# Kernel optimization log

Hardware: AMD Instinct MI355X
Metric: run time of the kernel (lower is better)

Reference implementation:

```python
import jax, jax.numpy as jnp
import numpy as np

N_NODES = 50000
N_EDGES = 400000
NODE_DIM = 128
EDGE_DIM = 64
HIDDEN = 128  # must equal NODE_DIM (index_add into zeros_like(node_feat))
EPS = 1e-8


def _param(key, shape):
    fan_in = shape[0]
    return (jax.random.normal(key, shape, jnp.float32) / np.sqrt(fan_in)).astype(jnp.float32)


def setup_inputs() -> dict:
    key = jax.random.key(0)
    ks = jax.random.split(key, 20)
    inp = {
        'node_feat': jax.random.normal(ks[0], (N_NODES, NODE_DIM), jnp.float32),
        'edge_attr': jax.random.normal(ks[1], (N_EDGES, EDGE_DIM), jnp.float32),
        'coords': 5.0 * jax.random.normal(ks[2], (N_NODES, 3), jnp.float32),
        'edge_index': jax.random.randint(ks[3], (2, N_EDGES), 0, N_NODES, dtype=jnp.int32),
        # edge_mlp: Linear(2*node+edge -> hidden), SiLU, Linear(hidden -> hidden), SiLU
        'We1': _param(ks[4], (2 * NODE_DIM + EDGE_DIM, HIDDEN)),
        'be1': jnp.zeros((HIDDEN,), jnp.float32),
        'We2': _param(ks[5], (HIDDEN, HIDDEN)),
        'be2': jnp.zeros((HIDDEN,), jnp.float32),
        # node_mlp: Linear(node+hidden -> hidden), SiLU, Linear(hidden -> node)
        'Wn1': _param(ks[6], (NODE_DIM + HIDDEN, HIDDEN)),
        'bn1': jnp.zeros((HIDDEN,), jnp.float32),
        'Wn2': _param(ks[7], (HIDDEN, NODE_DIM)),
        'bn2': jnp.zeros((NODE_DIM,), jnp.float32),
        # coord_mlp: Linear(hidden -> hidden//2), SiLU, Linear(hidden//2 -> 1)
        'Wc1': _param(ks[8], (HIDDEN, HIDDEN // 2)),
        'bc1': jnp.zeros((HIDDEN // 2,), jnp.float32),
        'Wc2': _param(ks[9], (HIDDEN // 2, 1)),
        'bc2': jnp.zeros((1,), jnp.float32),
    }
    return inp


def reference(node_feat, edge_attr, coords, edge_index,
              We1, be1, We2, be2,
              Wn1, bn1, Wn2, bn2,
              Wc1, bc1, Wc2, bc2):
    src, dst = edge_index[0], edge_index[1]
    n_nodes = node_feat.shape[0]

    # gather -> edge MLP
    edge_feat = jnp.concatenate([node_feat[src], node_feat[dst], edge_attr], axis=-1)  # [E, 2*ND+ED]
    edge_message = jax.nn.silu(jax.nn.silu(edge_feat @ We1 + be1) @ We2 + be2)         # [E, H]

    # scatter-add messages to destination nodes
    aggr = jax.ops.segment_sum(edge_message, dst, num_segments=n_nodes)                # [N, H]

    # node update (residual)
    node_in = jnp.concatenate([node_feat, aggr], axis=-1)
    node_update = jax.nn.silu(node_in @ Wn1 + bn1) @ Wn2 + bn2
    updated_nodes = node_feat + node_update

    # equivariant coordinate update
    coord_w = jax.nn.silu(edge_message @ Wc1 + bc1) @ Wc2 + bc2                        # [E, 1]
    coord_diff = coords[src] - coords[dst]                                             # [E, 3]
    coord_diff = coord_diff / (jnp.linalg.norm(coord_diff, axis=-1, keepdims=True) + EPS)
    coord_update = jax.ops.segment_sum(coord_w * coord_diff, dst, num_segments=n_nodes)
    updated_coords = coords + coord_update

    return (updated_nodes, updated_coords)
```

## Files before the change

### kernel.cpp

```cpp
#include <hip/hip_runtime.h>
#include <hip/hip_bf16.h>
#include <math.h>
#include <stdint.h>

#define NN 50000
#define NE 400000

typedef __attribute__((ext_vector_type(8))) short short8;
typedef __attribute__((ext_vector_type(4))) float f32x4;

#define OFF_WE1T 0
#define OFF_WE2T 40960
#define OFF_WN1T 57344
#define OFF_WN2T 90112
#define OFF_WC1T 106496
#define W_TOTAL  114688

#define NFB_ITEMS 800000
#define EAB_ITEMS 3200000

__device__ __forceinline__ float silu_f(float x) {
    return x * (1.0f / (1.0f + __expf(-x)));
}
__device__ __forceinline__ short f2bf(float f) {
    __hip_bfloat16 b = __float2bfloat16(f);
    return *reinterpret_cast<short*>(&b);
}
__device__ __forceinline__ short8 cvt8(float4 a, float4 b) {
    short8 r;
    r[0] = f2bf(a.x); r[1] = f2bf(a.y); r[2] = f2bf(a.z); r[3] = f2bf(a.w);
    r[4] = f2bf(b.x); r[5] = f2bf(b.y); r[6] = f2bf(b.z); r[7] = f2bf(b.w);
    return r;
}

__device__ __forceinline__ void gload16(const short* g, short* l) {
    __builtin_amdgcn_global_load_lds(
        (const __attribute__((address_space(1))) void*)g,
        (__attribute__((address_space(3))) void*)l, 16, 0, 0);
}

__global__ void zero_kernel(float4* __restrict__ p, int n4) {
    int i = blockIdx.x * blockDim.x + threadIdx.x;
    int st = gridDim.x * blockDim.x;
    for (; i < n4; i += st) p[i] = make_float4(0.f, 0.f, 0.f, 0.f);
}

__global__ __launch_bounds__(256) void prep_kernel(
    const float* __restrict__ We1, const float* __restrict__ We2,
    const float* __restrict__ Wn1, const float* __restrict__ Wn2,
    const float* __restrict__ Wc1, const float* __restrict__ nf,
    const float* __restrict__ ea,
    short* __restrict__ wb, short* __restrict__ nfb, short* __restrict__ eab,
    int full)
{
    const int i = blockIdx.x * 256 + threadIdx.x;
    if (i < W_TOTAL) {
        const float* src; int N, n, k, rel;
        if (i < OFF_WE2T)      { rel = i;            src = We1; N = 128; n = rel / 320; k = rel % 320; }
        else if (i < OFF_WN1T) { rel = i - OFF_WE2T; src = We2; N = 128; n = rel / 128; k = rel % 128; }
        else if (i < OFF_WN2T) { rel = i - OFF_WN1T; src = Wn1; N = 128; n = rel / 256; k = rel % 256; }
        else if (i < OFF_WC1T) { rel = i - OFF_WN2T; src = Wn2; N = 128; n = rel / 128; k = rel % 128; }
        else                   { rel = i - OFF_WC1T; src = Wc1; N = 64;  n = rel / 128; k = rel % 128; }
        wb[i] = f2bf(src[(size_t)k * N + n]);
    } else if (full && i < W_TOTAL + NFB_ITEMS) {
        const int j = i - W_TOTAL;
        const float4 a = *(const float4*)&nf[(size_t)j * 8];
        const float4 b = *(const float4*)&nf[(size_t)j * 8 + 4];
        *(short8*)&nfb[(size_t)j * 8] = cvt8(a, b);
    } else if (full && i < W_TOTAL + NFB_ITEMS + EAB_ITEMS) {
        const int j = i - W_TOTAL - NFB_ITEMS;
        const float4 a = *(const float4*)&ea[(size_t)j * 8];
        const float4 b = *(const float4*)&ea[(size_t)j * 8 + 4];
        *(short8*)&eab[(size_t)j * 8] = cvt8(a, b);
    }
}

template<bool STAGED>
__global__ __launch_bounds__(256, 2) void edge_kernel(
    const float* __restrict__ nf, const short* __restrict__ nfb,
    const float* __restrict__ ea, const short* __restrict__ eab,
    const float* __restrict__ coords, const int* __restrict__ ei,
    const short* __restrict__ wb,
    const float* __restrict__ be1, const float* __restrict__ be2,
    const float* __restrict__ bc1, const float* __restrict__ bc2,
    const float* __restrict__ Wc2f,
    float* __restrict__ aggr, float* __restrict__ coord_acc)
{
    __shared__ short smem[4][8192];

    const int tid = threadIdx.x;
    const int wv = tid >> 6, lane = tid & 63, le = lane & 15, g = lane >> 4;
    const int base = (blockIdx.x * 4 + wv) * 32;
    short* stage = smem[wv];
    short (*Hs)[136] = (short(*)[136])stage;

    const int s0 = ei[base + le],      s1 = ei[base + 16 + le];
    const int d0 = ei[NE + base + le], d1 = ei[NE + base + 16 + le];

    short8 ea8[2][2];
    if constexpr (STAGED) {
        #pragma unroll
        for (int kc = 0; kc < 8; ++kc) {
            const int r0 = (kc < 4) ? s0 : d0;
            const int r1 = (kc < 4) ? s1 : d1;
            const int col = (kc & 3) * 32 + g * 8;
            gload16(nfb + (size_t)r0 * 128 + col, stage + (kc * 2 + 0) * 512);
            gload16(nfb + (size_t)r1 * 128 + col, stage + (kc * 2 + 1) * 512);
        }
        #pragma unroll
        for (int q = 0; q < 2; ++q) {
            ea8[0][q] = *(const short8*)&eab[(size_t)(base + le) * 64 + q * 32 + g * 8];
            ea8[1][q] = *(const short8*)&eab[(size_t)(base + 16 + le) * 64 + q * 32 + g * 8];
        }
        asm volatile("s_waitcnt vmcnt(0)" ::: "memory");
        __builtin_amdgcn_sched_barrier(0);
    }

    f32x4 acc[2][8];
    #pragma unroll
    for (int m = 0; m < 2; ++m)
        #pragma unroll
        for (int t = 0; t < 8; ++t) acc[m][t] = (f32x4){0.f, 0.f, 0.f, 0.f};

    const short* w1 = wb + OFF_WE1T;
    #pragma unroll
    for (int kc = 0; kc < 10; ++kc) {
        const int gk = kc * 32 + g * 8;
        short8 a0, a1;
        if (kc < 8) {
            if constexpr (STAGED) {
                a0 = *(const short8*)&stage[(kc * 2 + 0) * 512 + lane * 8];
                a1 = *(const short8*)&stage[(kc * 2 + 1) * 512 + lane * 8];
            } else {
                const int r0 = (kc < 4) ? s0 : d0;
                const int r1 = (kc < 4) ? s1 : d1;
                const int col = (kc & 3) * 32 + g * 8;
                const float* p0 = nf + (size_t)r0 * 128 + col;
                const float* p1 = nf + (size_t)r1 * 128 + col;
                a0 = cvt8(*(const float4*)p0, *(const float4*)(p0 + 4));
                a1 = cvt8(*(const float4*)p1, *(const float4*)(p1 + 4));
            }
        } else {
            if constexpr (STAGED) {
                a0 = ea8[0][kc - 8];
                a1 = ea8[1][kc - 8];
            } else {
                const float* p0 = ea + (size_t)(base + le) * 64 + (kc - 8) * 32 + g * 8;
                const float* p1 = ea + (size_t)(base + 16 + le) * 64 + (kc - 8) * 32 + g * 8;
                a0 = cvt8(*(const float4*)p0, *(const float4*)(p0 + 4));
                a1 = cvt8(*(const float4*)p1, *(const float4*)(p1 + 4));
            }
        }
        short8 bfv[8];
        #pragma unroll
        for (int t = 0; t < 8; ++t)
            bfv[t] = *(const short8*)(w1 + (size_t)(t * 16 + le) * 320 + gk);
        #pragma unroll
        for (int t = 0; t < 8; ++t) {
            acc[0][t] = __builtin_amdgcn_mfma_f32_16x16x32_bf16(a0, bfv[t], acc[0][t], 0, 0, 0);
            acc[1][t] = __builtin_amdgcn_mfma_f32_16x16x32_bf16(a1, bfv[t], acc[1][t], 0, 0, 0);
        }
    }

    #pragma unroll
    for (int t = 0; t < 8; ++t) {
        const float b1 = be1[t * 16 + le];
        #pragma unroll
        for (int m = 0; m < 2; ++m)
            #pragma unroll
            for (int r = 0; r < 4; ++r)
                Hs[m * 16 + g * 4 + r][t * 16 + le] = f2bf(silu_f(acc[m][t][r] + b1));
    }

    f32x4 acc2[2][8];
    #pragma unroll
    for (int m = 0; m < 2; ++m)
        #pragma unroll
        for (int t = 0; t < 8; ++t) acc2[m][t] = (f32x4){0.f, 0.f, 0.f, 0.f};

    const short* w2 = wb + OFF_WE2T;
    #pragma unroll
    for (int kc = 0; kc < 4; ++kc) {
        const int gk = kc * 32 + g * 8;
        const short8 a0 = *(const short8*)&Hs[le][gk];
        const short8 a1 = *(const short8*)&Hs[16 + le][gk];
        short8 bfv[8];
        #pragma unroll
        for (int t = 0; t < 8; ++t)
            bfv[t] = *(const short8*)(w2 + (size_t)(t * 16 + le) * 128 + gk);
        #pragma unroll
        for (int t = 0; t < 8; ++t) {
            acc2[0][t] = __builtin_amdgcn_mfma_f32_16x16x32_bf16(a0, bfv[t], acc2[0][t], 0, 0, 0);
            acc2[1][t] = __builtin_amdgcn_mfma_f32_16x16x32_bf16(a1, bfv[t], acc2[1][t], 0, 0, 0);
        }
    }

    int dstv[2][4];
    #pragma unroll
    for (int r = 0; r < 4; ++r) {
        dstv[0][r] = __shfl(d0, g * 4 + r);
        dstv[1][r] = __shfl(d1, g * 4 + r);
    }
    #pragma unroll
    for (int t = 0; t < 8; ++t) {
        const float b2 = be2[t * 16 + le];
        #pragma unroll
        for (int m = 0; m < 2; ++m)
            #pragma unroll
            for (int r = 0; r < 4; ++r) {
                const float v = silu_f(acc2[m][t][r] + b2);
                atomicAdd(&aggr[(size_t)dstv[m][r] * 128 + t * 16 + le], v);
                Hs[m * 16 + g * 4 + r][t * 16 + le] = f2bf(v);
            }
    }

    f32x4 acc3[2][4];
    #pragma unroll
    for (int m = 0; m < 2; ++m)
        #pragma unroll
        for (int t = 0; t < 4; ++t) acc3[m][t] = (f32x4){0.f, 0.f, 0.f, 0.f};

    const short* wc = wb + OFF_WC1T;
    #pragma unroll
    for (int kc = 0; kc < 4; ++kc) {
        const int gk = kc * 32 + g * 8;
        const short8 a0 = *(const short8*)&Hs[le][gk];
        const short8 a1 = *(const short8*)&Hs[16 + le][gk];
        short8 bfv[4];
        #pragma unroll
        for (int t = 0; t < 4; ++t)
            bfv[t] = *(const short8*)(wc + (size_t)(t * 16 + le) * 128 + gk);
        #pragma unroll
        for (int t = 0; t < 4; ++t) {
            acc3[0][t] = __builtin_amdgcn_mfma_f32_16x16x32_bf16(a0, bfv[t], acc3[0][t], 0, 0, 0);
            acc3[1][t] = __builtin_amdgcn_mfma_f32_16x16x32_bf16(a1, bfv[t], acc3[1][t], 0, 0, 0);
        }
    }

    float part[2][4];
    #pragma unroll
    for (int m = 0; m < 2; ++m)
        #pragma unroll
        for (int r = 0; r < 4; ++r) part[m][r] = 0.f;
    #pragma unroll
    for (int t = 0; t < 4; ++t) {
        const float bc = bc1[t * 16 + le];
        const float w2c = Wc2f[t * 16 + le];
        #pragma unroll
        for (int m = 0; m < 2; ++m)
            #pragma unroll
            for (int r = 0; r < 4; ++r)
                part[m][r] += silu_f(acc3[m][t][r] + bc) * w2c;
    }
    #pragma unroll
    for (int mask = 1; mask <= 8; mask <<= 1)
        #pragma unroll
        for (int m = 0; m < 2; ++m)
            #pragma unroll
            for (int r = 0; r < 4; ++r)
                part[m][r] += __shfl_xor(part[m][r], mask);

    const int rr = le & 3;
    const int sA = __shfl(s0, g * 4 + rr), sB = __shfl(s1, g * 4 + rr);
    const int dA = __shfl(d0, g * 4 + rr), dB = __shfl(d1, g * 4 + rr);

    if (le < 8) {
        const int m = le >> 2, r = le & 3;
        float v;
        if (m == 0) v = (r == 0) ? part[0][0] : (r == 1) ? part[0][1] : (r == 2) ? part[0][2] : part[0][3];
        else        v = (r == 0) ? part[1][0] : (r == 1) ? part[1][1] : (r == 2) ? part[1][2] : part[1][3];
        const int s = m ? sB : sA, d = m ? dB : dA;
        const float dx = coords[3 * s + 0] - coords[3 * d + 0];
        const float dy = coords[3 * s + 1] - coords[3 * d + 1];
        const float dz = coords[3 * s + 2] - coords[3 * d + 2];
        const float wq = v + bc2[0];
        const float inv = wq / (sqrtf(dx * dx + dy * dy + dz * dz) + 1e-8f);
        atomicAdd(&coord_acc[3 * d + 0], dx * inv);
        atomicAdd(&coord_acc[3 * d + 1], dy * inv);
        atomicAdd(&coord_acc[3 * d + 2], dz * inv);
    }
}

template<bool BF16NF>
__global__ __launch_bounds__(256, 2) void node_kernel(
    const float* __restrict__ nf, const short* __restrict__ nfb,
    const float* __restrict__ coords, const short* __restrict__ wb,
    const float* __restrict__ bn1, const float* __restrict__ bn2,
    const float* __restrict__ aggr, const float* __restrict__ coord_acc,
    float* __restrict__ out)
{
    __shared__ short Hs[128][136];

    const int tid = threadIdx.x;
    const int wv = tid >> 6, lane = tid & 63, le = lane & 15, grp = lane >> 4;
    const int nb = blockIdx.x * 128, wbase = wv * 32;
    const int row0 = min(nb + wbase + le, NN - 1);
    const int row1 = min(nb + wbase + 16 + le, NN - 1);

    f32x4 acc[2][8];
    #pragma unroll
    for (int m = 0; m < 2; ++m)
        #pragma unroll
        for (int t = 0; t < 8; ++t) acc[m][t] = (f32x4){0.f, 0.f, 0.f, 0.f};

    const short* w1 = wb + OFF_WN1T;
    #pragma unroll
    for (int kc = 0; kc < 8; ++kc) {
        const int gk = kc * 32 + grp * 8;
        short8 a0, a1;
        if (kc < 4) {
            if (BF16NF) {
                a0 = *(const short8*)&nfb[(size_t)row0 * 128 + gk];
                a1 = *(const short8*)&nfb[(size_t)row1 * 128 + gk];
            } else {
                const float* p0 = nf + (size_t)row0 * 128 + gk;
                const float* p1 = nf + (size_t)row1 * 128 + gk;
                a0 = cvt8(*(const float4*)p0, *(const float4*)(p0 + 4));
                a1 = cvt8(*(const float4*)p1, *(const float4*)(p1 + 4));
            }
        } else {
            const float* p0 = aggr + (size_t)row0 * 128 + gk - 128;
            const float* p1 = aggr + (size_t)row1 * 128 + gk - 128;
            a0 = cvt8(*(const float4*)p0, *(const float4*)(p0 + 4));
            a1 = cvt8(*(const float4*)p1, *(const float4*)(p1 + 4));
        }
        short8 bfv[8];
        #pragma unroll
        for (int t = 0; t < 8; ++t)
            bfv[t] = *(const short8*)(w1 + (size_t)(t * 16 + le) * 256 + gk);
        #pragma unroll
        for (int t = 0; t < 8; ++t) {
            acc[0][t] = __builtin_amdgcn_mfma_f32_16x16x32_bf16(a0, bfv[t], acc[0][t], 0, 0, 0);
            acc[1][t] = __builtin_amdgcn_mfma_f32_16x16x32_bf16(a1, bfv[t], acc[1][t], 0, 0, 0);
        }
    }
    #pragma unroll
    for (int t = 0; t < 8; ++t) {
        const float b1 = bn1[t * 16 + le];
        #pragma unroll
        for (int m = 0; m < 2; ++m)
            #pragma unroll
            for (int r = 0; r < 4; ++r)
                Hs[wbase + m * 16 + grp * 4 + r][t * 16 + le] = f2bf(silu_f(acc[m][t][r] + b1));
    }

    f32x4 acc2[2][8];
    #pragma unroll
    for (int m = 0; m < 2; ++m)
        #pragma unroll
        for (int t = 0; t < 8; ++t) acc2[m][t] = (f32x4){0.f, 0.f, 0.f, 0.f};

    const short* w2 = wb + OFF_WN2T;
    #pragma unroll
    for (int kc = 0; kc < 4; ++kc) {
        const int gk = kc * 32 + grp * 8;
        const short8 a0 = *(const short8*)&Hs[wbase + le][gk];
        const short8 a1 = *(const short8*)&Hs[wbase + 16 + le][gk];
        short8 bfv[8];
        #pragma unroll
        for (int t = 0; t < 8; ++t)
            bfv[t] = *(const short8*)(w2 + (size_t)(t * 16 + le) * 128 + gk);
        #pragma unroll
        for (int t = 0; t < 8; ++t) {
            acc2[0][t] = __builtin_amdgcn_mfma_f32_16x16x32_bf16(a0, bfv[t], acc2[0][t], 0, 0, 0);
            acc2[1][t] = __builtin_amdgcn_mfma_f32_16x16x32_bf16(a1, bfv[t], acc2[1][t], 0, 0, 0);
        }
    }
    #pragma unroll
    for (int t = 0; t < 8; ++t) {
        const float b2 = bn2[t * 16 + le];
        #pragma unroll
        for (int m = 0; m < 2; ++m)
            #pragma unroll
            for (int r = 0; r < 4; ++r) {
                const int row = nb + wbase + m * 16 + grp * 4 + r;
                if (row < NN) {
                    const int c = t * 16 + le;
                    out[(size_t)row * 128 + c] = acc2[m][t][r] + b2 + nf[(size_t)row * 128 + c];
                }
            }
    }

    for (int i = tid; i < 384; i += 256) {
        const int n = nb + i / 3, j = i % 3;
        if (n < NN)
            out[(size_t)NN * 128 + 3 * n + j] = coords[3 * n + j] + coord_acc[3 * n + j];
    }
}

extern "C" void kernel_launch(void* const* d_in, const int* in_sizes, int n_in,
                              void* d_out, int out_size, void* d_ws, size_t ws_size,
                              hipStream_t stream)
{
    const float* node_feat  = (const float*)d_in[0];
    const float* edge_attr  = (const float*)d_in[1];
    const float* coords     = (const float*)d_in[2];
    const int*   edge_index = (const int*)d_in[3];
    const float* We1 = (const float*)d_in[4];
    const float* be1 = (const float*)d_in[5];
    const float* We2 = (const float*)d_in[6];
    const float* be2 = (const float*)d_in[7];
    const float* Wn1 = (const float*)d_in[8];
    const float* bn1 = (const float*)d_in[9];
    const float* Wn2 = (const float*)d_in[10];
    const float* bn2 = (const float*)d_in[11];
    const float* Wc1 = (const float*)d_in[12];
    const float* bc1 = (const float*)d_in[13];
    const float* Wc2 = (const float*)d_in[14];
    const float* bc2 = (const float*)d_in[15];
    float* out = (float*)d_out;

    const size_t sz_wb   = (size_t)W_TOTAL * 2;
    const size_t sz_agg  = (size_t)NN * 128 * 4;
    const size_t sz_cac  = (size_t)NN * 3 * 4;
    const size_t sz_nfb  = (size_t)NN * 128 * 2;
    const size_t sz_eab  = (size_t)NE * 64 * 2;
    const size_t need_full = sz_wb + sz_agg + sz_cac + sz_nfb + sz_eab;
    const size_t need_min  = sz_wb + sz_agg + sz_cac;

    char* p = (char*)d_ws;
    short* wbf       = (short*)p;  p += sz_wb;
    float* aggr      = (float*)p;  p += sz_agg;
    float* coord_acc = (float*)p;  p += sz_cac;
    short* nfb       = (short*)p;  p += sz_nfb;
    short* eab       = (short*)p;

    const int n4 = (NN * 128 + NN * 3) / 4;
    const int eg = NE / 128;
    const int ng = (NN + 127) / 128;

    if (ws_size >= need_full) {
        const int pg = (W_TOTAL + NFB_ITEMS + EAB_ITEMS + 255) / 256;
        prep_kernel<<<pg, 256, 0, stream>>>(
            We1, We2, Wn1, Wn2, Wc1, node_feat, edge_attr, wbf, nfb, eab, 1);
        zero_kernel<<<2048, 256, 0, stream>>>((float4*)aggr, n4);

        edge_kernel<true><<<eg, 256, 0, stream>>>(
            node_feat, nfb, edge_attr, eab, coords, edge_index, wbf,
            be1, be2, bc1, bc2, Wc2, aggr, coord_acc);

        node_kernel<true><<<ng, 256, 0, stream>>>(
            node_feat, nfb, coords, wbf, bn1, bn2, aggr, coord_acc, out);
    } else {
        const int pg = (W_TOTAL + 255) / 256;
        prep_kernel<<<pg, 256, 0, stream>>>(
            We1, We2, Wn1, Wn2, Wc1, node_feat, edge_attr, wbf, nullptr, nullptr, 0);
        zero_kernel<<<2048, 256, 0, stream>>>((float4*)aggr, n4);

        edge_kernel<false><<<eg, 256, 0, stream>>>(
            node_feat, nullptr, edge_attr, nullptr, coords, edge_index, wbf,
            be1, be2, bc1, bc2, Wc2, aggr, coord_acc);

        node_kernel<false><<<ng, 256, 0, stream>>>(
            node_feat, nullptr, coords, wbf, bn1, bn2, aggr, coord_acc, out);
    }
}
```

Baseline: 405.1 us.

## Halve edges per wave, raise occupancy, drop edge_attr bf16 pre-conversion

The edge kernel now has each wave handle 16 edges instead of 32. Per-wave shared staging and accumulator register arrays shrink, and launch bounds rise from 2 to 5 blocks per CU to hide gather latency. The separate prep pass that converted edge_attr to bf16 is removed, and edge attributes are read as fp32 and converted in registers, which saves a full write and re-read of that tensor. In exchange, each weight fragment loaded from global memory feeds only one MFMA instead of two, which doubles weight-load traffic per edge.

```diff
diff --git a/kernel.cpp b/kernel.cpp
--- a/kernel.cpp
+++ b/kernel.cpp
@@ -17,7 +17,6 @@
 #define W_TOTAL  114688
 
 #define NFB_ITEMS 800000
-#define EAB_ITEMS 3200000
 
 __device__ __forceinline__ float silu_f(float x) {
     return x * (1.0f / (1.0f + __expf(-x)));
@@ -49,9 +48,7 @@
     const float* __restrict__ We1, const float* __restrict__ We2,
     const float* __restrict__ Wn1, const float* __restrict__ Wn2,
     const float* __restrict__ Wc1, const float* __restrict__ nf,
-    const float* __restrict__ ea,
-    short* __restrict__ wb, short* __restrict__ nfb, short* __restrict__ eab,
-    int full)
+    short* __restrict__ wb, short* __restrict__ nfb, int full)
 {
     const int i = blockIdx.x * 256 + threadIdx.x;
     if (i < W_TOTAL) {
@@ -67,18 +64,13 @@
         const float4 a = *(const float4*)&nf[(size_t)j * 8];
         const float4 b = *(const float4*)&nf[(size_t)j * 8 + 4];
         *(short8*)&nfb[(size_t)j * 8] = cvt8(a, b);
-    } else if (full && i < W_TOTAL + NFB_ITEMS + EAB_ITEMS) {
-        const int j = i - W_TOTAL - NFB_ITEMS;
-        const float4 a = *(const float4*)&ea[(size_t)j * 8];
-        const float4 b = *(const float4*)&ea[(size_t)j * 8 + 4];
-        *(short8*)&eab[(size_t)j * 8] = cvt8(a, b);
     }
 }
 
 template<bool STAGED>
-__global__ __launch_bounds__(256, 2) void edge_kernel(
+__global__ __launch_bounds__(256, 5) void edge_kernel(
     const float* __restrict__ nf, const short* __restrict__ nfb,
-    const float* __restrict__ ea, const short* __restrict__ eab,
+    const float* __restrict__ ea,
     const float* __restrict__ coords, const int* __restrict__ ei,
     const short* __restrict__ wb,
     const float* __restrict__ be1, const float* __restrict__ be2,
@@ -86,198 +78,155 @@
     const float* __restrict__ Wc2f,
     float* __restrict__ aggr, float* __restrict__ coord_acc)
 {
-    __shared__ short smem[4][8192];
+    __shared__ short smem[4][4096];
 
     const int tid = threadIdx.x;
     const int wv = tid >> 6, lane = tid & 63, le = lane & 15, g = lane >> 4;
-    const int base = (blockIdx.x * 4 + wv) * 32;
+    const int base = (blockIdx.x * 4 + wv) * 16;
     short* stage = smem[wv];
     short (*Hs)[136] = (short(*)[136])stage;
 
-    const int s0 = ei[base + le],      s1 = ei[base + 16 + le];
-    const int d0 = ei[NE + base + le], d1 = ei[NE + base + 16 + le];
-
-    short8 ea8[2][2];
+    const int s0 = ei[base + le];
+    const int d0 = ei[NE + base + le];
+
     if constexpr (STAGED) {
         #pragma unroll
         for (int kc = 0; kc < 8; ++kc) {
             const int r0 = (kc < 4) ? s0 : d0;
-            const int r1 = (kc < 4) ? s1 : d1;
-            const int col = (kc & 3) * 32 + g * 8;
-            gload16(nfb + (size_t)r0 * 128 + col, stage + (kc * 2 + 0) * 512);
-            gload16(nfb + (size_t)r1 * 128 + col, stage + (kc * 2 + 1) * 512);
-        }
-        #pragma unroll
-        for (int q = 0; q < 2; ++q) {
-            ea8[0][q] = *(const short8*)&eab[(size_t)(base + le) * 64 + q * 32 + g * 8];
-            ea8[1][q] = *(const short8*)&eab[(size_t)(base + 16 + le) * 64 + q * 32 + g * 8];
-        }
+            gload16(nfb + (size_t)r0 * 128 + (kc & 3) * 32 + g * 8, stage + kc * 512);
+        }
+    }
+    float4 eaf[2][2];
+    #pragma unroll
+    for (int q = 0; q < 2; ++q) {
+        const float* pe = ea + (size_t)(base + le) * 64 + q * 32 + g * 8;
+        eaf[q][0] = *(const float4*)pe;
+        eaf[q][1] = *(const float4*)(pe + 4);
+    }
+    if constexpr (STAGED) {
         asm volatile("s_waitcnt vmcnt(0)" ::: "memory");
         __builtin_amdgcn_sched_barrier(0);
     }
 
-    f32x4 acc[2][8];
-    #pragma unroll
-    for (int m = 0; m < 2; ++m)
-        #pragma unroll
-        for (int t = 0; t < 8; ++t) acc[m][t] = (f32x4){0.f, 0.f, 0.f, 0.f};
+    f32x4 acc[8];
+    #pragma unroll
+    for (int t = 0; t < 8; ++t) acc[t] = (f32x4){0.f, 0.f, 0.f, 0.f};
 
     const short* w1 = wb + OFF_WE1T;
     #pragma unroll
     for (int kc = 0; kc < 10; ++kc) {
         const int gk = kc * 32 + g * 8;
-        short8 a0, a1;
+        short8 a0;
         if (kc < 8) {
             if constexpr (STAGED) {
-                a0 = *(const short8*)&stage[(kc * 2 + 0) * 512 + lane * 8];
-                a1 = *(const short8*)&stage[(kc * 2 + 1) * 512 + lane * 8];
+                a0 = *(const short8*)&stage[kc * 512 + lane * 8];
             } else {
                 const int r0 = (kc < 4) ? s0 : d0;
-                const int r1 = (kc < 4) ? s1 : d1;
-                const int col = (kc & 3) * 32 + g * 8;
-                const float* p0 = nf + (size_t)r0 * 128 + col;
-                const float* p1 = nf + (size_t)r1 * 128 + col;
+                const float* p0 = nf + (size_t)r0 * 128 + (kc & 3) * 32 + g * 8;
                 a0 = cvt8(*(const float4*)p0, *(const float4*)(p0 + 4));
-                a1 = cvt8(*(const float4*)p1, *(const float4*)(p1 + 4));
             }
         } else {
-            if constexpr (STAGED) {
-                a0 = ea8[0][kc - 8];
-                a1 = ea8[1][kc - 8];
-            } else {
-                const float* p0 = ea + (size_t)(base + le) * 64 + (kc - 8) * 32 + g * 8;
-                const float* p1 = ea + (size_t)(base + 16 + le) * 64 + (kc - 8) * 32 + g * 8;
-                a0 = cvt8(*(const float4*)p0, *(const float4*)(p0 + 4));
-                a1 = cvt8(*(const float4*)p1, *(const float4*)(p1 + 4));
-            }
+            a0 = cvt8(eaf[kc - 8][0], eaf[kc - 8][1]);
         }
         short8 bfv[8];
         #pragma unroll
         for (int t = 0; t < 8; ++t)
             bfv[t] = *(const short8*)(w1 + (size_t)(t * 16 + le) * 320 + gk);
         #pragma unroll
-        for (int t = 0; t < 8; ++t) {
-            acc[0][t] = __builtin_amdgcn_mfma_f32_16x16x32_bf16(a0, bfv[t], acc[0][t], 0, 0, 0);
-            acc[1][t] = __builtin_amdgcn_mfma_f32_16x16x32_bf16(a1, bfv[t], acc[1][t], 0, 0, 0);
-        }
+        for (int t = 0; t < 8; ++t)
+            acc[t] = __builtin_amdgcn_mfma_f32_16x16x32_bf16(a0, bfv[t], acc[t], 0, 0, 0);
     }
 
     #pragma unroll
     for (int t = 0; t < 8; ++t) {
         const float b1 = be1[t * 16 + le];
         #pragma unroll
-        for (int m = 0; m < 2; ++m)
-            #pragma unroll
-            for (int r = 0; r < 4; ++r)
-                Hs[m * 16 + g * 4 + r][t * 16 + le] = f2bf(silu_f(acc[m][t][r] + b1));
-    }
-
-    f32x4 acc2[2][8];
-    #pragma unroll
-    for (int m = 0; m < 2; ++m)
-        #pragma unroll
-        for (int t = 0; t < 8; ++t) acc2[m][t] = (f32x4){0.f, 0.f, 0.f, 0.f};
+        for (int r = 0; r < 4; ++r)
+            Hs[g * 4 + r][t * 16 + le] = f2bf(silu_f(acc[t][r] + b1));
+    }
+
+    f32x4 acc2[8];
+    #pragma unroll
+    for (int t = 0; t < 8; ++t) acc2[t] = (f32x4){0.f, 0.f, 0.f, 0.f};
 
     const short* w2 = wb + OFF_WE2T;
     #pragma unroll
     for (int kc = 0; kc < 4; ++kc) {
         const int gk = kc * 32 + g * 8;
         const short8 a0 = *(const short8*)&Hs[le][gk];
-        const short8 a1 = *(const short8*)&Hs[16 + le][gk];
         short8 bfv[8];
         #pragma unroll
         for (int t = 0; t < 8; ++t)
             bfv[t] = *(const short8*)(w2 + (size_t)(t * 16 + le) * 128 + gk);
         #pragma unroll
-        for (int t = 0; t < 8; ++t) {
-            acc2[0][t] = __builtin_amdgcn_mfma_f32_16x16x32_bf16(a0, bfv[t], acc2[0][t], 0, 0, 0);
-            acc2[1][t] = __builtin_amdgcn_mfma_f32_16x16x32_bf16(a1, bfv[t], acc2[1][t], 0, 0, 0);
-        }
-    }
-
-    int dstv[2][4];
-    #pragma unroll
-    for (int r = 0; r < 4; ++r) {
-        dstv[0][r] = __shfl(d0, g * 4 + r);
-        dstv[1][r] = __shfl(d1, g * 4 + r);
-    }
+        for (int t = 0; t < 8; ++t)
+            acc2[t] = __builtin_amdgcn_mfma_f32_16x16x32_bf16(a0, bfv[t], acc2[t], 0, 0, 0);
+    }
+
+    int dstv[4];
+    #pragma unroll
+    for (int r = 0; r < 4; ++r) dstv[r] = __shfl(d0, g * 4 + r);
+
     #pragma unroll
     for (int t = 0; t < 8; ++t) {
         const float b2 = be2[t * 16 + le];
         #pragma unroll
-        for (int m = 0; m < 2; ++m)
-            #pragma unroll
-            for (int r = 0; r < 4; ++r) {
-                const float v = silu_f(acc2[m][t][r] + b2);
-                atomicAdd(&aggr[(size_t)dstv[m][r] * 128 + t * 16 + le], v);
-                Hs[m * 16 + g * 4 + r][t * 16 + le] = f2bf(v);
-            }
-    }
-
-    f32x4 acc3[2][4];
-    #pragma unroll
-    for (int m = 0; m < 2; ++m)
-        #pragma unroll
-        for (int t = 0; t < 4; ++t) acc3[m][t] = (f32x4){0.f, 0.f, 0.f, 0.f};
+        for (int r = 0; r < 4; ++r) {
+            const float v = silu_f(acc2[t][r] + b2);
+            atomicAdd(&aggr[(size_t)dstv[r] * 128 + t * 16 + le], v);
+            Hs[g * 4 + r][t * 16 + le] = f2bf(v);
+        }
+    }
+
+    f32x4 acc3[4];
+    #pragma unroll
+    for (int t = 0; t < 4; ++t) acc3[t] = (f32x4){0.f, 0.f, 0.f, 0.f};
 
     const short* wc = wb + OFF_WC1T;
     #pragma unroll
     for (int kc = 0; kc < 4; ++kc) {
         const int gk = kc * 32 + g * 8;
         const short8 a0 = *(const short8*)&Hs[le][gk];
-        const short8 a1 = *(const short8*)&Hs[16 + le][gk];
         short8 bfv[4];
         #pragma unroll
         for (int t = 0; t < 4; ++t)
             bfv[t] = *(const short8*)(wc + (size_t)(t * 16 + le) * 128 + gk);
         #pragma unroll
-        for (int t = 0; t < 4; ++t) {
-            acc3[0][t] = __builtin_amdgcn_mfma_f32_16x16x32_bf16(a0, bfv[t], acc3[0][t], 0, 0, 0);
-            acc3[1][t] = __builtin_amdgcn_mfma_f32_16x16x32_bf16(a1, bfv[t], acc3[1][t], 0, 0, 0);
-        }
-    }
-
-    float part[2][4];
-    #pragma unroll
-    for (int m = 0; m < 2; ++m)
-        #pragma unroll
-        for (int r = 0; r < 4; ++r) part[m][r] = 0.f;
+        for (int t = 0; t < 4; ++t)
+            acc3[t] = __builtin_amdgcn_mfma_f32_16x16x32_bf16(a0, bfv[t], acc3[t], 0, 0, 0);
+    }
+
+    float part[4];
+    #pragma unroll
+    for (int r = 0; r < 4; ++r) part[r] = 0.f;
     #pragma unroll
     for (int t = 0; t < 4; ++t) {
         const float bc = bc1[t * 16 + le];
         const float w2c = Wc2f[t * 16 + le];
         #pragma unroll
-        for (int m = 0; m < 2; ++m)
-            #pragma unroll
-            for (int r = 0; r < 4; ++r)
-                part[m][r] += silu_f(acc3[m][t][r] + bc) * w2c;
+        for (int r = 0; r < 4; ++r)
+            part[r] += silu_f(acc3[t][r] + bc) * w2c;
     }
     #pragma unroll
     for (int mask = 1; mask <= 8; mask <<= 1)
         #pragma unroll
-        for (int m = 0; m < 2; ++m)
-            #pragma unroll
-            for (int r = 0; r < 4; ++r)
-                part[m][r] += __shfl_xor(part[m][r], mask);
+        for (int r = 0; r < 4; ++r)
+            part[r] += __shfl_xor(part[r], mask);
 
     const int rr = le & 3;
-    const int sA = __shfl(s0, g * 4 + rr), sB = __shfl(s1, g * 4 + rr);
-    const int dA = __shfl(d0, g * 4 + rr), dB = __shfl(d1, g * 4 + rr);
-
-    if (le < 8) {
-        const int m = le >> 2, r = le & 3;
-        float v;
-        if (m == 0) v = (r == 0) ? part[0][0] : (r == 1) ? part[0][1] : (r == 2) ? part[0][2] : part[0][3];
-        else        v = (r == 0) ? part[1][0] : (r == 1) ? part[1][1] : (r == 2) ? part[1][2] : part[1][3];
-        const int s = m ? sB : sA, d = m ? dB : dA;
-        const float dx = coords[3 * s + 0] - coords[3 * d + 0];
-        const float dy = coords[3 * s + 1] - coords[3 * d + 1];
-        const float dz = coords[3 * s + 2] - coords[3 * d + 2];
+    const int sA = __shfl(s0, g * 4 + rr);
+    const int dA = __shfl(d0, g * 4 + rr);
+
+    if (le < 4) {
+        const float v = (rr == 0) ? part[0] : (rr == 1) ? part[1] : (rr == 2) ? part[2] : part[3];
+        const float dx = coords[3 * sA + 0] - coords[3 * dA + 0];
+        const float dy = coords[3 * sA + 1] - coords[3 * dA + 1];
+        const float dz = coords[3 * sA + 2] - coords[3 * dA + 2];
         const float wq = v + bc2[0];
         const float inv = wq / (sqrtf(dx * dx + dy * dy + dz * dz) + 1e-8f);
-        atomicAdd(&coord_acc[3 * d + 0], dx * inv);
-        atomicAdd(&coord_acc[3 * d + 1], dy * inv);
-        atomicAdd(&coord_acc[3 * d + 2], dz * inv);
+        atomicAdd(&coord_acc[3 * dA + 0], dx * inv);
+        atomicAdd(&coord_acc[3 * dA + 1], dy * inv);
+        atomicAdd(&coord_acc[3 * dA + 2], dz * inv);
     }
 }
 
@@ -414,29 +363,27 @@
     const size_t sz_agg  = (size_t)NN * 128 * 4;
     const size_t sz_cac  = (size_t)NN * 3 * 4;
     const size_t sz_nfb  = (size_t)NN * 128 * 2;
-    const size_t sz_eab  = (size_t)NE * 64 * 2;
-    const size_t need_full = sz_wb + sz_agg + sz_cac + sz_nfb + sz_eab;
-    const size_t need_min  = sz_wb + sz_agg + sz_cac;
+    const size_t need_full = sz_wb + sz_agg + sz_cac + sz_nfb;
+    (void)need_full;
 
     char* p = (char*)d_ws;
     short* wbf       = (short*)p;  p += sz_wb;
     float* aggr      = (float*)p;  p += sz_agg;
     float* coord_acc = (float*)p;  p += sz_cac;
-    short* nfb       = (short*)p;  p += sz_nfb;
-    short* eab       = (short*)p;
+    short* nfb       = (short*)p;
 
     const int n4 = (NN * 128 + NN * 3) / 4;
-    const int eg = NE / 128;
+    const int eg = NE / 64;
     const int ng = (NN + 127) / 128;
 
     if (ws_size >= need_full) {
-        const int pg = (W_TOTAL + NFB_ITEMS + EAB_ITEMS + 255) / 256;
+        const int pg = (W_TOTAL + NFB_ITEMS + 255) / 256;
         prep_kernel<<<pg, 256, 0, stream>>>(
-            We1, We2, Wn1, Wn2, Wc1, node_feat, edge_attr, wbf, nfb, eab, 1);
+            We1, We2, Wn1, Wn2, Wc1, node_feat, wbf, nfb, 1);
         zero_kernel<<<2048, 256, 0, stream>>>((float4*)aggr, n4);
 
         edge_kernel<true><<<eg, 256, 0, stream>>>(
-            node_feat, nfb, edge_attr, eab, coords, edge_index, wbf,
+            node_feat, nfb, edge_attr, coords, edge_index, wbf,
             be1, be2, bc1, bc2, Wc2, aggr, coord_acc);
 
         node_kernel<true><<<ng, 256, 0, stream>>>(
@@ -444,11 +391,11 @@
     } else {
         const int pg = (W_TOTAL + 255) / 256;
         prep_kernel<<<pg, 256, 0, stream>>>(
-            We1, We2, Wn1, Wn2, Wc1, node_feat, edge_attr, wbf, nullptr, nullptr, 0);
+            We1, We2, Wn1, Wn2, Wc1, node_feat, wbf, nullptr, 0);
         zero_kernel<<<2048, 256, 0, stream>>>((float4*)aggr, n4);
 
         edge_kernel<false><<<eg, 256, 0, stream>>>(
-            node_feat, nullptr, edge_attr, nullptr, coords, edge_index, wbf,
+            node_feat, nullptr, edge_attr, coords, edge_index, wbf,
             be1, be2, bc1, bc2, Wc2, aggr, coord_acc);
 
         node_kernel<false><<<ng, 256, 0, stream>>>(
```

After: 537.9 us. +32.8%, slower.

## Precompute per-node first-layer projections and gather them instead of raw features

Applied to the files above, without the earlier changes.

The first edge-MLP layer is split algebraically: node_feat@We1_src and node_feat@We1_dst are computed once per node in a new ynode kernel and stored as bf16, and the edge kernel gathers these projections and adds them to the edge_attr projection. This removes most of the per-edge first-layer MFMA work (256 of 320 K columns) and drops the bf16 prep conversion of node/edge features. The cost is an extra node-level GEMM pass, an extra bf16 rounding of the partial sums, two gathers of 128-wide bf16 rows per edge, and removal of the workspace-size fallback path.

```diff
diff --git a/kernel.cpp b/kernel.cpp
--- a/kernel.cpp
+++ b/kernel.cpp
@@ -9,22 +9,25 @@
 typedef __attribute__((ext_vector_type(8))) short short8;
 typedef __attribute__((ext_vector_type(4))) float f32x4;
 
-#define OFF_WE1T 0
+#define OFF_W1S  0
+#define OFF_W1D  16384
+#define OFF_W1E  32768
 #define OFF_WE2T 40960
 #define OFF_WN1T 57344
 #define OFF_WN2T 90112
 #define OFF_WC1T 106496
 #define W_TOTAL  114688
 
-#define NFB_ITEMS 800000
-#define EAB_ITEMS 3200000
-
 __device__ __forceinline__ float silu_f(float x) {
     return x * (1.0f / (1.0f + __expf(-x)));
 }
 __device__ __forceinline__ short f2bf(float f) {
     __hip_bfloat16 b = __float2bfloat16(f);
     return *reinterpret_cast<short*>(&b);
+}
+__device__ __forceinline__ float bf2f(short s) {
+    uint32_t u = ((uint32_t)(uint16_t)s) << 16;
+    float f; __builtin_memcpy(&f, &u, 4); return f;
 }
 __device__ __forceinline__ short8 cvt8(float4 a, float4 b) {
     short8 r;
@@ -48,39 +51,76 @@
 __global__ __launch_bounds__(256) void prep_kernel(
     const float* __restrict__ We1, const float* __restrict__ We2,
     const float* __restrict__ Wn1, const float* __restrict__ Wn2,
-    const float* __restrict__ Wc1, const float* __restrict__ nf,
-    const float* __restrict__ ea,
-    short* __restrict__ wb, short* __restrict__ nfb, short* __restrict__ eab,
-    int full)
+    const float* __restrict__ Wc1, short* __restrict__ wb)
 {
     const int i = blockIdx.x * 256 + threadIdx.x;
-    if (i < W_TOTAL) {
-        const float* src; int N, n, k, rel;
-        if (i < OFF_WE2T)      { rel = i;            src = We1; N = 128; n = rel / 320; k = rel % 320; }
-        else if (i < OFF_WN1T) { rel = i - OFF_WE2T; src = We2; N = 128; n = rel / 128; k = rel % 128; }
-        else if (i < OFF_WN2T) { rel = i - OFF_WN1T; src = Wn1; N = 128; n = rel / 256; k = rel % 256; }
-        else if (i < OFF_WC1T) { rel = i - OFF_WN2T; src = Wn2; N = 128; n = rel / 128; k = rel % 128; }
-        else                   { rel = i - OFF_WC1T; src = Wc1; N = 64;  n = rel / 128; k = rel % 128; }
-        wb[i] = f2bf(src[(size_t)k * N + n]);
-    } else if (full && i < W_TOTAL + NFB_ITEMS) {
-        const int j = i - W_TOTAL;
-        const float4 a = *(const float4*)&nf[(size_t)j * 8];
-        const float4 b = *(const float4*)&nf[(size_t)j * 8 + 4];
-        *(short8*)&nfb[(size_t)j * 8] = cvt8(a, b);
-    } else if (full && i < W_TOTAL + NFB_ITEMS + EAB_ITEMS) {
-        const int j = i - W_TOTAL - NFB_ITEMS;
-        const float4 a = *(const float4*)&ea[(size_t)j * 8];
-        const float4 b = *(const float4*)&ea[(size_t)j * 8 + 4];
-        *(short8*)&eab[(size_t)j * 8] = cvt8(a, b);
-    }
-}
-
-template<bool STAGED>
+    if (i >= W_TOTAL) return;
+    float v; int rel, n, k;
+    if (i < OFF_W1D)       { rel = i;            n = rel >> 7; k = rel & 127; v = We1[k * 128 + n]; }
+    else if (i < OFF_W1E)  { rel = i - OFF_W1D;  n = rel >> 7; k = rel & 127; v = We1[(k + 128) * 128 + n]; }
+    else if (i < OFF_WE2T) { rel = i - OFF_W1E;  n = rel >> 6; k = rel & 63;  v = We1[(k + 256) * 128 + n]; }
+    else if (i < OFF_WN1T) { rel = i - OFF_WE2T; n = rel >> 7; k = rel & 127; v = We2[k * 128 + n]; }
+    else if (i < OFF_WN2T) { rel = i - OFF_WN1T; n = rel >> 8; k = rel & 255; v = Wn1[k * 128 + n]; }
+    else if (i < OFF_WC1T) { rel = i - OFF_WN2T; n = rel >> 7; k = rel & 127; v = Wn2[k * 128 + n]; }
+    else                   { rel = i - OFF_WC1T; n = rel >> 7; k = rel & 127; v = Wc1[k * 64 + n]; }
+    wb[i] = f2bf(v);
+}
+
+__global__ __launch_bounds__(256, 4) void ynode_kernel(
+    const float* __restrict__ nf, const short* __restrict__ wb,
+    short* __restrict__ ysb, short* __restrict__ ydb)
+{
+    const int tid = threadIdx.x;
+    const int wv = tid >> 6, lane = tid & 63, le = lane & 15, grp = lane >> 4;
+    const int nb = blockIdx.x * 128, wbase = wv * 32;
+    const int row0 = min(nb + wbase + le, NN - 1);
+    const int row1 = min(nb + wbase + 16 + le, NN - 1);
+
+    #pragma unroll 1
+    for (int pass = 0; pass < 2; ++pass) {
+        const short* wt = wb + (pass ? OFF_W1D : OFF_W1S);
+        short* op = pass ? ydb : ysb;
+
+        f32x4 acc[2][8];
+        #pragma unroll
+        for (int m = 0; m < 2; ++m)
+            #pragma unroll
+            for (int t = 0; t < 8; ++t) acc[m][t] = (f32x4){0.f, 0.f, 0.f, 0.f};
+
+        #pragma unroll
+        for (int kc = 0; kc < 4; ++kc) {
+            const int gk = kc * 32 + grp * 8;
+            const float* p0 = nf + (size_t)row0 * 128 + gk;
+            const float* p1 = nf + (size_t)row1 * 128 + gk;
+            const short8 a0 = cvt8(*(const float4*)p0, *(const float4*)(p0 + 4));
+            const short8 a1 = cvt8(*(const float4*)p1, *(const float4*)(p1 + 4));
+            short8 bfv[8];
+            #pragma unroll
+            for (int t = 0; t < 8; ++t)
+                bfv[t] = *(const short8*)(wt + (size_t)(t * 16 + le) * 128 + gk);
+            #pragma unroll
+            for (int t = 0; t < 8; ++t) {
+                acc[0][t] = __builtin_amdgcn_mfma_f32_16x16x32_bf16(a0, bfv[t], acc[0][t], 0, 0, 0);
+                acc[1][t] = __builtin_amdgcn_mfma_f32_16x16x32_bf16(a1, bfv[t], acc[1][t], 0, 0, 0);
+            }
+        }
+        #pragma unroll
+        for (int t = 0; t < 8; ++t)
+            #pragma unroll
+            for (int m = 0; m < 2; ++m)
+                #pragma unroll
+                for (int r = 0; r < 4; ++r) {
+                    const int row = nb + wbase + m * 16 + grp * 4 + r;
+                    if (row < NN)
+                        op[(size_t)row * 128 + t * 16 + le] = f2bf(acc[m][t][r]);
+                }
+    }
+}
+
 __global__ __launch_bounds__(256, 2) void edge_kernel(
-    const float* __restrict__ nf, const short* __restrict__ nfb,
-    const float* __restrict__ ea, const short* __restrict__ eab,
-    const float* __restrict__ coords, const int* __restrict__ ei,
-    const short* __restrict__ wb,
+    const short* __restrict__ ysb, const short* __restrict__ ydb,
+    const float* __restrict__ ea, const float* __restrict__ coords,
+    const int* __restrict__ ei, const short* __restrict__ wb,
     const float* __restrict__ be1, const float* __restrict__ be2,
     const float* __restrict__ bc1, const float* __restrict__ bc2,
     const float* __restrict__ Wc2f,
@@ -92,28 +132,16 @@
     const int wv = tid >> 6, lane = tid & 63, le = lane & 15, g = lane >> 4;
     const int base = (blockIdx.x * 4 + wv) * 32;
     short* stage = smem[wv];
-    short (*Hs)[136] = (short(*)[136])stage;
 
     const int s0 = ei[base + le],      s1 = ei[base + 16 + le];
     const int d0 = ei[NE + base + le], d1 = ei[NE + base + 16 + le];
 
-    short8 ea8[2][2];
-    if constexpr (STAGED) {
-        #pragma unroll
-        for (int kc = 0; kc < 8; ++kc) {
-            const int r0 = (kc < 4) ? s0 : d0;
-            const int r1 = (kc < 4) ? s1 : d1;
-            const int col = (kc & 3) * 32 + g * 8;
-            gload16(nfb + (size_t)r0 * 128 + col, stage + (kc * 2 + 0) * 512);
-            gload16(nfb + (size_t)r1 * 128 + col, stage + (kc * 2 + 1) * 512);
-        }
-        #pragma unroll
-        for (int q = 0; q < 2; ++q) {
-            ea8[0][q] = *(const short8*)&eab[(size_t)(base + le) * 64 + q * 32 + g * 8];
-            ea8[1][q] = *(const short8*)&eab[(size_t)(base + 16 + le) * 64 + q * 32 + g * 8];
-        }
-        asm volatile("s_waitcnt vmcnt(0)" ::: "memory");
-        __builtin_amdgcn_sched_barrier(0);
+    #pragma unroll
+    for (int q = 0; q < 4; ++q) {
+        gload16(ysb + (size_t)s0 * 128 + q * 32 + g * 8, stage + q * 512);
+        gload16(ysb + (size_t)s1 * 128 + q * 32 + g * 8, stage + 2048 + q * 512);
+        gload16(ydb + (size_t)d0 * 128 + q * 32 + g * 8, stage + 4096 + q * 512);
+        gload16(ydb + (size_t)d1 * 128 + q * 32 + g * 8, stage + 6144 + q * 512);
     }
 
     f32x4 acc[2][8];
@@ -122,39 +150,18 @@
         #pragma unroll
         for (int t = 0; t < 8; ++t) acc[m][t] = (f32x4){0.f, 0.f, 0.f, 0.f};
 
-    const short* w1 = wb + OFF_WE1T;
-    #pragma unroll
-    for (int kc = 0; kc < 10; ++kc) {
+    const short* w1e = wb + OFF_W1E;
+    #pragma unroll
+    for (int kc = 0; kc < 2; ++kc) {
         const int gk = kc * 32 + g * 8;
-        short8 a0, a1;
-        if (kc < 8) {
-            if constexpr (STAGED) {
-                a0 = *(const short8*)&stage[(kc * 2 + 0) * 512 + lane * 8];
-                a1 = *(const short8*)&stage[(kc * 2 + 1) * 512 + lane * 8];
-            } else {
-                const int r0 = (kc < 4) ? s0 : d0;
-                const int r1 = (kc < 4) ? s1 : d1;
-                const int col = (kc & 3) * 32 + g * 8;
-                const float* p0 = nf + (size_t)r0 * 128 + col;
-                const float* p1 = nf + (size_t)r1 * 128 + col;
-                a0 = cvt8(*(const float4*)p0, *(const float4*)(p0 + 4));
-                a1 = cvt8(*(const float4*)p1, *(const float4*)(p1 + 4));
-            }
-        } else {
-            if constexpr (STAGED) {
-                a0 = ea8[0][kc - 8];
-                a1 = ea8[1][kc - 8];
-            } else {
-                const float* p0 = ea + (size_t)(base + le) * 64 + (kc - 8) * 32 + g * 8;
-                const float* p1 = ea + (size_t)(base + 16 + le) * 64 + (kc - 8) * 32 + g * 8;
-                a0 = cvt8(*(const float4*)p0, *(const float4*)(p0 + 4));
-                a1 = cvt8(*(const float4*)p1, *(const float4*)(p1 + 4));
-            }
-        }
+        const float* p0 = ea + (size_t)(base + le) * 64 + gk;
+        const float* p1 = ea + (size_t)(base + 16 + le) * 64 + gk;
+        const short8 a0 = cvt8(*(const float4*)p0, *(const float4*)(p0 + 4));
+        const short8 a1 = cvt8(*(const float4*)p1, *(const float4*)(p1 + 4));
         short8 bfv[8];
         #pragma unroll
         for (int t = 0; t < 8; ++t)
-            bfv[t] = *(const short8*)(w1 + (size_t)(t * 16 + le) * 320 + gk);
+            bfv[t] = *(const short8*)(w1e + (size_t)(t * 16 + le) * 64 + gk);
         #pragma unroll
         for (int t = 0; t < 8; ++t) {
             acc[0][t] = __builtin_amdgcn_mfma_f32_16x16x32_bf16(a0, bfv[t], acc[0][t], 0, 0, 0);
@@ -162,14 +169,22 @@
         }
     }
 
+    asm volatile("s_waitcnt vmcnt(0)" ::: "memory");
+    __builtin_amdgcn_sched_barrier(0);
+
     #pragma unroll
     for (int t = 0; t < 8; ++t) {
-        const float b1 = be1[t * 16 + le];
-        #pragma unroll
-        for (int m = 0; m < 2; ++m)
-            #pragma unroll
-            for (int r = 0; r < 4; ++r)
-                Hs[m * 16 + g * 4 + r][t * 16 + le] = f2bf(silu_f(acc[m][t][r] + b1));
+        const int col = t * 16 + le;
+        const float b1 = be1[col];
+        const int c8 = col >> 3, q = c8 >> 2, cc = c8 & 3, el = col & 7;
+        #pragma unroll
+        for (int m = 0; m < 2; ++m)
+            #pragma unroll
+            for (int r = 0; r < 4; ++r) {
+                const int ad = m * 2048 + q * 512 + cc * 128 + (g * 4 + r) * 8 + el;
+                const float v = silu_f(acc[m][t][r] + bf2f(stage[ad]) + bf2f(stage[4096 + ad]) + b1);
+                stage[ad] = f2bf(v);
+            }
     }
 
     f32x4 acc2[2][8];
@@ -182,8 +197,8 @@
     #pragma unroll
     for (int kc = 0; kc < 4; ++kc) {
         const int gk = kc * 32 + g * 8;
-        const short8 a0 = *(const short8*)&Hs[le][gk];
-        const short8 a1 = *(const short8*)&Hs[16 + le][gk];
+        const short8 a0 = *(const short8*)&stage[kc * 512 + g * 128 + le * 8];
+        const short8 a1 = *(const short8*)&stage[2048 + kc * 512 + g * 128 + le * 8];
         short8 bfv[8];
         #pragma unroll
         for (int t = 0; t < 8; ++t)
@@ -203,14 +218,16 @@
     }
     #pragma unroll
     for (int t = 0; t < 8; ++t) {
-        const float b2 = be2[t * 16 + le];
+        const int col = t * 16 + le;
+        const float b2 = be2[col];
+        const int c8 = col >> 3, q = c8 >> 2, cc = c8 & 3, el = col & 7;
         #pragma unroll
         for (int m = 0; m < 2; ++m)
             #pragma unroll
             for (int r = 0; r < 4; ++r) {
                 const float v = silu_f(acc2[m][t][r] + b2);
-                atomicAdd(&aggr[(size_t)dstv[m][r] * 128 + t * 16 + le], v);
-                Hs[m * 16 + g * 4 + r][t * 16 + le] = f2bf(v);
+                atomicAdd(&aggr[(size_t)dstv[m][r] * 128 + col], v);
+                stage[4096 + m * 2048 + q * 512 + cc * 128 + (g * 4 + r) * 8 + el] = f2bf(v);
             }
     }
 
@@ -224,8 +241,8 @@
     #pragma unroll
     for (int kc = 0; kc < 4; ++kc) {
         const int gk = kc * 32 + g * 8;
-        const short8 a0 = *(const short8*)&Hs[le][gk];
-        const short8 a1 = *(const short8*)&Hs[16 + le][gk];
+        const short8 a0 = *(const short8*)&stage[4096 + kc * 512 + g * 128 + le * 8];
+        const short8 a1 = *(const short8*)&stage[6144 + kc * 512 + g * 128 + le * 8];
         short8 bfv[4];
         #pragma unroll
         for (int t = 0; t < 4; ++t)
@@ -281,10 +298,9 @@
     }
 }
 
-template<bool BF16NF>
 __global__ __launch_bounds__(256, 2) void node_kernel(
-    const float* __restrict__ nf, const short* __restrict__ nfb,
-    const float* __restrict__ coords, const short* __restrict__ wb,
+    const float* __restrict__ nf, const float* __restrict__ coords,
+    const short* __restrict__ wb,
     const float* __restrict__ bn1, const float* __restrict__ bn2,
     const float* __restrict__ aggr, const float* __restrict__ coord_acc,
     float* __restrict__ out)
@@ -307,23 +323,10 @@
     #pragma unroll
     for (int kc = 0; kc < 8; ++kc) {
         const int gk = kc * 32 + grp * 8;
-        short8 a0, a1;
-        if (kc < 4) {
-            if (BF16NF) {
-                a0 = *(const short8*)&nfb[(size_t)row0 * 128 + gk];
-                a1 = *(const short8*)&nfb[(size_t)row1 * 128 + gk];
-            } else {
-                const float* p0 = nf + (size_t)row0 * 128 + gk;
-                const float* p1 = nf + (size_t)row1 * 128 + gk;
-                a0 = cvt8(*(const float4*)p0, *(const float4*)(p0 + 4));
-                a1 = cvt8(*(const float4*)p1, *(const float4*)(p1 + 4));
-            }
-        } else {
-            const float* p0 = aggr + (size_t)row0 * 128 + gk - 128;
-            const float* p1 = aggr + (size_t)row1 * 128 + gk - 128;
-            a0 = cvt8(*(const float4*)p0, *(const float4*)(p0 + 4));
-            a1 = cvt8(*(const float4*)p1, *(const float4*)(p1 + 4));
-        }
+        const float* p0 = (kc < 4) ? nf + (size_t)row0 * 128 + gk : aggr + (size_t)row0 * 128 + gk - 128;
+        const float* p1 = (kc < 4) ? nf + (size_t)row1 * 128 + gk : aggr + (size_t)row1 * 128 + gk - 128;
+        const short8 a0 = cvt8(*(const float4*)p0, *(const float4*)(p0 + 4));
+        const short8 a1 = cvt8(*(const float4*)p1, *(const float4*)(p1 + 4));
         short8 bfv[8];
         #pragma unroll
         for (int t = 0; t < 8; ++t)
@@ -410,48 +413,31 @@
     const float* bc2 = (const float*)d_in[15];
     float* out = (float*)d_out;
 
-    const size_t sz_wb   = (size_t)W_TOTAL * 2;
-    const size_t sz_agg  = (size_t)NN * 128 * 4;
-    const size_t sz_cac  = (size_t)NN * 3 * 4;
-    const size_t sz_nfb  = (size_t)NN * 128 * 2;
-    const size_t sz_eab  = (size_t)NE * 64 * 2;
-    const size_t need_full = sz_wb + sz_agg + sz_cac + sz_nfb + sz_eab;
-    const size_t need_min  = sz_wb + sz_agg + sz_cac;
+    const size_t sz_wb  = (size_t)W_TOTAL * 2;
+    const size_t sz_agg = (size_t)NN * 128 * 4;
+    const size_t sz_cac = (size_t)NN * 3 * 4;
+    const size_t sz_y   = (size_t)NN * 128 * 2;
 
     char* p = (char*)d_ws;
     short* wbf       = (short*)p;  p += sz_wb;
     float* aggr      = (float*)p;  p += sz_agg;
     float* coord_acc = (float*)p;  p += sz_cac;
-    short* nfb       = (short*)p;  p += sz_nfb;
-    short* eab       = (short*)p;
+    short* ysb       = (short*)p;  p += sz_y;
+    short* ydb       = (short*)p;
+    (void)ws_size;
 
     const int n4 = (NN * 128 + NN * 3) / 4;
     const int eg = NE / 128;
     const int ng = (NN + 127) / 128;
 
-    if (ws_size >= need_full) {
-        const int pg = (W_TOTAL + NFB_ITEMS + EAB_ITEMS + 255) / 256;
-        prep_kernel<<<pg, 256, 0, stream>>>(
-            We1, We2, Wn1, Wn2, Wc1, node_feat, edge_attr, wbf, nfb, eab, 1);
-        zero_kernel<<<2048, 256, 0, stream>>>((float4*)aggr, n4);
-
-        edge_kernel<true><<<eg, 256, 0, stream>>>(
-            node_feat, nfb, edge_attr, eab, coords, edge_index, wbf,
-            be1, be2, bc1, bc2, Wc2, aggr, coord_acc);
-
-        node_kernel<true><<<ng, 256, 0, stream>>>(
-            node_feat, nfb, coords, wbf, bn1, bn2, aggr, coord_acc, out);
-    } else {
-        const int pg = (W_TOTAL + 255) / 256;
-        prep_kernel<<<pg, 256, 0, stream>>>(
-            We1, We2, Wn1, Wn2, Wc1, node_feat, edge_attr, wbf, nullptr, nullptr, 0);
-        zero_kernel<<<2048, 256, 0, stream>>>((float4*)aggr, n4);
-
-        edge_kernel<false><<<eg, 256, 0, stream>>>(
-            node_feat, nullptr, edge_attr, nullptr, coords, edge_index, wbf,
-            be1, be2, bc1, bc2, Wc2, aggr, coord_acc);
-
-        node_kernel<false><<<ng, 256, 0, stream>>>(
-            node_feat, nullptr, coords, wbf, bn1, bn2, aggr, coord_acc, out);
-    }
-}
+    prep_kernel<<<(W_TOTAL + 255) / 256, 256, 0, stream>>>(We1, We2, Wn1, Wn2, Wc1, wbf);
+    zero_kernel<<<2048, 256, 0, stream>>>((float4*)aggr, n4);
+    ynode_kernel<<<ng, 256, 0, stream>>>(node_feat, wbf, ysb, ydb);
+
+    edge_kernel<<<eg, 256, 0, stream>>>(
+        ysb, ydb, edge_attr, coords, edge_index, wbf,
+        be1, be2, bc1, bc2, Wc2, aggr, coord_acc);
+
+    node_kernel<<<ng, 256, 0, stream>>>(
+        node_feat, coords, wbf, bn1, bn2, aggr, coord_acc, out);
+}
```

Measured after the change: 390.0 us. 1.04x faster.
